# Performance work log

Hardware: AMD Instinct MI355X
Metric: run time of the kernel (lower is better)

## Reference

```python
import jax, jax.numpy as jnp
import numpy as np

N_NODES = 40000
N_EDGES = 640000
D = 128  # in_channels == out_channels (required by the module's math)


def setup_inputs() -> dict:
    key = jax.random.key(0)
    ks = jax.random.split(key, 8)
    s = 1.0 / np.sqrt(D)  # torch Linear default init scale
    x = jax.random.normal(ks[0], (N_NODES, D), dtype=jnp.float32)
    edge_index = jax.random.randint(ks[1], (2, N_EDGES), 0, N_NODES, dtype=jnp.int64)
    Wn_w = jax.random.uniform(ks[2], (D, D), jnp.float32, -s, s)
    Wn_b = jax.random.uniform(ks[3], (D,), jnp.float32, -s, s)
    Wg_w = jax.random.uniform(ks[4], (D, D), jnp.float32, -s, s)
    Wg_b = jax.random.uniform(ks[5], (D,), jnp.float32, -s, s)
    Wa_w = jax.random.uniform(ks[6], (D, D), jnp.float32, -s, s)
    Wa_b = jax.random.uniform(ks[7], (D,), jnp.float32, -s, s)
    return {"x": x, "edge_index": edge_index,
            "Wn_w": Wn_w, "Wn_b": Wn_b,
            "Wg_w": Wg_w, "Wg_b": Wg_b,
            "Wa_w": Wa_w, "Wa_b": Wa_b}


def reference(x, edge_index, Wn_w, Wn_b, Wg_w, Wg_b, Wa_w, Wa_b):
    row, col = edge_index[0], edge_index[1]
    x_col = x[col]                                  # [E, D] gather
    alpha = jax.nn.sigmoid(x_col @ Wa_w + Wa_b)     # [E, D] edge attention
    neigh = x_col * alpha                           # [E, D]
    aggr = jax.ops.segment_sum(neigh, row, num_segments=x.shape[0])  # [N, D]
    out = jnp.tanh((x @ Wn_w + Wn_b) + (aggr @ Wg_w + Wg_b))
    return out  # dropout p=0.0 is identity
```

## Files before the change

kernel.cpp:

```cpp
#include <hip/hip_runtime.h>

#define NN 40000
#define NE 640000
#define D 128
#define CAP 64

typedef __attribute__((ext_vector_type(8))) short short8;
typedef __attribute__((ext_vector_type(4))) float f32x4;
typedef __attribute__((ext_vector_type(4))) int i32x4;

__device__ __forceinline__ short f2b(float v) {
  unsigned int u = __builtin_bit_cast(unsigned int, v);
  u = (u + 0x7fffu + ((u >> 16) & 1u)) >> 16;
  return (short)u;
}
__device__ __forceinline__ float b2f(short s) {
  unsigned int u = ((unsigned int)(unsigned short)s) << 16;
  return __builtin_bit_cast(float, u);
}

__global__ __launch_bounds__(256) void k_prep(
    const float* __restrict__ Wn, const float* __restrict__ Wg,
    const float* __restrict__ Wa, short* __restrict__ WnT,
    short* __restrict__ WgThi, short* __restrict__ WgTlo,
    short* __restrict__ WaT, int* __restrict__ cnt, short* __restrict__ h) {
  int i = blockIdx.x * 256 + threadIdx.x;
  int k = i >> 7, c = i & 127;
  WnT[c * D + k] = f2b(Wn[k * D + c]);
  WaT[c * D + k] = f2b(Wa[k * D + c]);
  float v = Wg[k * D + c];
  short hi = f2b(v);
  WgThi[c * D + k] = hi;
  WgTlo[c * D + k] = f2b(v - b2f(hi));
  if (i < 10000) {
    i32x4 z = {0, 0, 0, 0};
    *(i32x4*)(cnt + i * 4) = z;
  }
  if (i < 16) {
    short8 z = {0, 0, 0, 0, 0, 0, 0, 0};
    *(short8*)(h + (size_t)NN * D + i * 8) = z;
  }
}

__global__ __launch_bounds__(256) void k_fill(
    const int* __restrict__ ei, int* __restrict__ cnt,
    unsigned short* __restrict__ bucket) {
  int e = blockIdx.x * 256 + threadIdx.x;
  if (e >= NE) return;
  int r = ei[e];
  int c = ei[NE + e];
  int slot = atomicAdd(&cnt[r], 1);
  if (slot < CAP) bucket[(size_t)r * CAP + slot] = (unsigned short)c;
}

__global__ __launch_bounds__(256) void k_node(
    const float* __restrict__ x, const short* __restrict__ WaT,
    const float* __restrict__ ba, short* __restrict__ h_out,
    short* __restrict__ xbf_out) {
  __shared__ float xs[16][132];
  __shared__ float al_s[16][132];
  int r0 = blockIdx.x * 16;
  int t = threadIdx.x;
  int w = t >> 6, l = t & 63;
  int g = l >> 4, c16 = l & 15;

#pragma unroll
  for (int p = 0; p < 2; ++p) {
    int idx = t + p * 256;
    int row = idx >> 5, cv = idx & 31;
    f32x4 v = *(const f32x4*)(x + (size_t)(r0 + row) * D + cv * 4);
    *(f32x4*)&xs[row][cv * 4] = v;
  }
  __syncthreads();

  short8 a[4];
#pragma unroll
  for (int kt = 0; kt < 4; ++kt) {
    f32x4 v0 = *(const f32x4*)&xs[c16][kt * 32 + g * 8];
    f32x4 v1 = *(const f32x4*)&xs[c16][kt * 32 + g * 8 + 4];
    short8 tt;
    tt[0] = f2b(v0[0]); tt[1] = f2b(v0[1]); tt[2] = f2b(v0[2]); tt[3] = f2b(v0[3]);
    tt[4] = f2b(v1[0]); tt[5] = f2b(v1[1]); tt[6] = f2b(v1[2]); tt[7] = f2b(v1[3]);
    a[kt] = tt;
    *(short8*)(xbf_out + (size_t)(r0 + c16) * D + kt * 32 + g * 8) = tt;
  }

#pragma unroll
  for (int u = 0; u < 2; ++u) {
    int ct = w * 2 + u;
    int cc = ct * 16 + c16;
    f32x4 c = {0.f, 0.f, 0.f, 0.f};
#pragma unroll
    for (int kt = 0; kt < 4; ++kt) {
      short8 b = *(const short8*)(WaT + (size_t)cc * D + kt * 32 + g * 8);
      c = __builtin_amdgcn_mfma_f32_16x16x32_bf16(a[kt], b, c, 0, 0, 0);
    }
    float bav = ba[cc];
#pragma unroll
    for (int r = 0; r < 4; ++r) {
      float tv = c[r] + bav;
      al_s[g * 4 + r][cc] = 1.0f / (1.0f + __expf(-tv));
    }
  }
  __syncthreads();

  short8 hh;
#pragma unroll
  for (int q = 0; q < 8; ++q) {
    float av = al_s[c16][w * 32 + g * 8 + q];
    float xv = xs[c16][w * 32 + g * 8 + q];
    hh[q] = f2b(xv * av);
  }
  *(short8*)(h_out + (size_t)(r0 + c16) * D + w * 32 + g * 8) = hh;
}

#define PSTEP(T0, C0A, C0B, C1A, C1B)                               \
  {                                                                 \
    int s0 = 4 * (T0) + g, s1 = s0 + 4;                             \
    int ra0 = s0 < deg0 ? (C0A) : NN;                               \
    int ra1 = s1 < deg0 ? (C0B) : NN;                               \
    int rb0 = s0 < deg1 ? (C1A) : NN;                               \
    int rb1 = s1 < deg1 ? (C1B) : NN;                               \
    short8 va0 = *(const short8*)(h + (size_t)ra0 * D + i * 8);     \
    short8 va1 = *(const short8*)(h + (size_t)ra1 * D + i * 8);     \
    short8 vb0 = *(const short8*)(h + (size_t)rb0 * D + i * 8);     \
    short8 vb1 = *(const short8*)(h + (size_t)rb1 * D + i * 8);     \
    _Pragma("unroll") for (int q = 0; q < 8; ++q) {                 \
      a0[q] += b2f(va0[q]) + b2f(va1[q]);                           \
      a1[q] += b2f(vb0[q]) + b2f(vb1[q]);                           \
    }                                                               \
  }

__global__ __launch_bounds__(512) void k_fused(
    const int* __restrict__ cnt, const unsigned short* __restrict__ bucket,
    const short* __restrict__ h, const short* __restrict__ xbf,
    const short* __restrict__ WnT, const short* __restrict__ WgThi,
    const short* __restrict__ WgTlo, const float* __restrict__ bn,
    const float* __restrict__ bg, float* __restrict__ out) {
  __shared__ float st[16][132];
  __shared__ short xsb[16][132];
  int w = threadIdx.x >> 6, l = threadIdx.x & 63;
  int g = l >> 4, i = l & 15;
  int base = blockIdx.x * 16;

  if (threadIdx.x < 256) {
    int idx = threadIdx.x;
    int row = idx >> 4, ch = idx & 15;
    *(short8*)&xsb[row][ch * 8] =
        *(const short8*)(xbf + (size_t)(base + row) * D + ch * 8);
  }

  {
    int n0 = base + 2 * w, n1 = n0 + 1;
    int deg0 = cnt[n0]; deg0 = deg0 < CAP ? deg0 : CAP;
    int deg1 = cnt[n1]; deg1 = deg1 < CAP ? deg1 : CAP;
    int dmax = deg0 > deg1 ? deg0 : deg1;
    int bc0 = bucket[(size_t)n0 * CAP + l];
    int bc1 = bucket[(size_t)n1 * CAP + l];
    float a0[8], a1[8];
#pragma unroll
    for (int q = 0; q < 8; ++q) { a0[q] = 0.f; a1[q] = 0.f; }

    int c00 = __shfl(bc0, g), c01 = __shfl(bc0, 4 + g);
    int c02 = __shfl(bc0, 8 + g), c03 = __shfl(bc0, 12 + g);
    int c10 = __shfl(bc1, g), c11 = __shfl(bc1, 4 + g);
    int c12 = __shfl(bc1, 8 + g), c13 = __shfl(bc1, 12 + g);
    PSTEP(0, c00, c01, c10, c11);
    if (dmax > 8) PSTEP(2, c02, c03, c12, c13);
    if (dmax > 16) {
      int c04 = __shfl(bc0, 16 + g), c05 = __shfl(bc0, 20 + g);
      int c14 = __shfl(bc1, 16 + g), c15 = __shfl(bc1, 20 + g);
      PSTEP(4, c04, c05, c14, c15);
    }
    if (dmax > 24) {
      int c06 = __shfl(bc0, 24 + g), c07 = __shfl(bc0, 28 + g);
      int c16_ = __shfl(bc1, 24 + g), c17 = __shfl(bc1, 28 + g);
      PSTEP(6, c06, c07, c16_, c17);
    }
    if (dmax > 32) {
      for (int j = 32; j < dmax; j += 8) {
        int s0 = j + g, s1 = j + 4 + g;
        int d00 = __shfl(bc0, s0 & 63), d01 = __shfl(bc0, s1 & 63);
        int d10 = __shfl(bc1, s0 & 63), d11 = __shfl(bc1, s1 & 63);
        int ra0 = s0 < deg0 ? d00 : NN;
        int ra1 = s1 < deg0 ? d01 : NN;
        int rb0 = s0 < deg1 ? d10 : NN;
        int rb1 = s1 < deg1 ? d11 : NN;
        short8 va0 = *(const short8*)(h + (size_t)ra0 * D + i * 8);
        short8 va1 = *(const short8*)(h + (size_t)ra1 * D + i * 8);
        short8 vb0 = *(const short8*)(h + (size_t)rb0 * D + i * 8);
        short8 vb1 = *(const short8*)(h + (size_t)rb1 * D + i * 8);
#pragma unroll
        for (int q = 0; q < 8; ++q) {
          a0[q] += b2f(va0[q]) + b2f(va1[q]);
          a1[q] += b2f(vb0[q]) + b2f(vb1[q]);
        }
      }
    }
#pragma unroll
    for (int q = 0; q < 8; ++q) {
      a0[q] += __shfl_xor(a0[q], 16);
      a0[q] += __shfl_xor(a0[q], 32);
      a1[q] += __shfl_xor(a1[q], 16);
      a1[q] += __shfl_xor(a1[q], 32);
    }
    if (g == 0) {
      f32x4 lo = {a0[0], a0[1], a0[2], a0[3]};
      f32x4 hi = {a0[4], a0[5], a0[6], a0[7]};
      *(f32x4*)&st[w * 2][i * 8] = lo;
      *(f32x4*)&st[w * 2][i * 8 + 4] = hi;
    } else if (g == 1) {
      f32x4 lo = {a1[0], a1[1], a1[2], a1[3]};
      f32x4 hi = {a1[4], a1[5], a1[6], a1[7]};
      *(f32x4*)&st[w * 2 + 1][i * 8] = lo;
      *(f32x4*)&st[w * 2 + 1][i * 8 + 4] = hi;
    }
  }
  __syncthreads();

  int cc = w * 16 + i;
  f32x4 c = {0.f, 0.f, 0.f, 0.f};
  float bias = bn[cc] + bg[cc];
#pragma unroll
  for (int kt = 0; kt < 4; ++kt) {
    short8 axf = *(const short8*)&xsb[i][kt * 32 + g * 8];
    const float* p = &st[i][kt * 32 + g * 8];
    f32x4 v0 = *(const f32x4*)p;
    f32x4 v1 = *(const f32x4*)(p + 4);
    short8 sh, sl;
#pragma unroll
    for (int jq = 0; jq < 4; ++jq) {
      short hh = f2b(v0[jq]);
      sh[jq] = hh;
      sl[jq] = f2b(v0[jq] - b2f(hh));
    }
#pragma unroll
    for (int jq = 0; jq < 4; ++jq) {
      short hh = f2b(v1[jq]);
      sh[4 + jq] = hh;
      sl[4 + jq] = f2b(v1[jq] - b2f(hh));
    }
    short8 bwn = *(const short8*)(WnT + (size_t)cc * D + kt * 32 + g * 8);
    short8 bh = *(const short8*)(WgThi + (size_t)cc * D + kt * 32 + g * 8);
    short8 bl = *(const short8*)(WgTlo + (size_t)cc * D + kt * 32 + g * 8);
    c = __builtin_amdgcn_mfma_f32_16x16x32_bf16(axf, bwn, c, 0, 0, 0);
    c = __builtin_amdgcn_mfma_f32_16x16x32_bf16(sh, bh, c, 0, 0, 0);
    c = __builtin_amdgcn_mfma_f32_16x16x32_bf16(sl, bh, c, 0, 0, 0);
    c = __builtin_amdgcn_mfma_f32_16x16x32_bf16(sh, bl, c, 0, 0, 0);
  }
#pragma unroll
  for (int r = 0; r < 4; ++r) {
    int rr = base + g * 4 + r;
    out[(size_t)rr * D + cc] = tanhf(c[r] + bias);
  }
}

extern "C" void kernel_launch(void* const* d_in, const int* in_sizes, int n_in,
                              void* d_out, int out_size, void* d_ws,
                              size_t ws_size, hipStream_t stream) {
  const float* x = (const float*)d_in[0];
  const int* ei = (const int*)d_in[1];
  const float* Wn_w = (const float*)d_in[2];
  const float* Wn_b = (const float*)d_in[3];
  const float* Wg_w = (const float*)d_in[4];
  const float* Wg_b = (const float*)d_in[5];
  const float* Wa_w = (const float*)d_in[6];
  const float* Wa_b = (const float*)d_in[7];

  char* ws = (char*)d_ws;
  short* WaT = (short*)(ws + 0);
  short* WnT = (short*)(ws + 32 * 1024);
  short* WgThi = (short*)(ws + 64 * 1024);
  short* WgTlo = (short*)(ws + 96 * 1024);
  int* cnt = (int*)(ws + 128 * 1024);
  size_t off = 512 * 1024;
  short* h = (short*)(ws + off);
  off += (size_t)(NN + 1) * D * 2;
  short* xbf = (short*)(ws + off);
  off += (size_t)NN * D * 2;
  unsigned short* bucket = (unsigned short*)(ws + off);
  float* out = (float*)d_out;

  k_prep<<<64, 256, 0, stream>>>(Wn_w, Wg_w, Wa_w, WnT, WgThi, WgTlo, WaT,
                                 cnt, h);
  k_fill<<<(NE + 255) / 256, 256, 0, stream>>>(ei, cnt, bucket);
  k_node<<<NN / 16, 256, 0, stream>>>(x, WaT, Wa_b, h, xbf);
  k_fused<<<2500, 512, 0, stream>>>(cnt, bucket, h, xbf, WnT, WgThi, WgTlo,
                                    Wn_b, Wg_b, out);
}
```

Baseline: 107.0 us.

## Double rows per block with dynamic node-pair scheduling across waves

Each block of k_fused now handles 32 nodes instead of 16. Waves pull node pairs from a shared atomic counter, so uneven node degrees are balanced within the block instead of each wave owning a fixed pair. The epilogue is restructured so each wave computes two 16-column tiles for one 16-row tile, reusing the converted A fragments across both. This halves the block count and adds LDS atomics, and the larger LDS footprint may lower occupancy.

```diff
diff --git a/kernel.cpp b/kernel.cpp
--- a/kernel.cpp
+++ b/kernel.cpp
@@ -137,21 +137,24 @@
     const short* __restrict__ WnT, const short* __restrict__ WgThi,
     const short* __restrict__ WgTlo, const float* __restrict__ bn,
     const float* __restrict__ bg, float* __restrict__ out) {
-  __shared__ float st[16][132];
-  __shared__ short xsb[16][132];
+  __shared__ float st[32][132];
+  __shared__ short xsb[32][132];
+  __shared__ int nxt;
   int w = threadIdx.x >> 6, l = threadIdx.x & 63;
   int g = l >> 4, i = l & 15;
-  int base = blockIdx.x * 16;
-
-  if (threadIdx.x < 256) {
-    int idx = threadIdx.x;
-    int row = idx >> 4, ch = idx & 15;
+  int base = blockIdx.x * 32;
+
+  {
+    int row = threadIdx.x >> 4, ch = threadIdx.x & 15;
     *(short8*)&xsb[row][ch * 8] =
         *(const short8*)(xbf + (size_t)(base + row) * D + ch * 8);
   }
-
-  {
-    int n0 = base + 2 * w, n1 = n0 + 1;
+  if (threadIdx.x == 0) nxt = 8;
+  __syncthreads();
+
+  int p = w;
+  while (true) {
+    int n0 = base + 2 * p, n1 = n0 + 1;
     int deg0 = cnt[n0]; deg0 = deg0 < CAP ? deg0 : CAP;
     int deg1 = cnt[n1]; deg1 = deg1 < CAP ? deg1 : CAP;
     int dmax = deg0 > deg1 ? deg0 : deg1;
@@ -207,51 +210,69 @@
     if (g == 0) {
       f32x4 lo = {a0[0], a0[1], a0[2], a0[3]};
       f32x4 hi = {a0[4], a0[5], a0[6], a0[7]};
-      *(f32x4*)&st[w * 2][i * 8] = lo;
-      *(f32x4*)&st[w * 2][i * 8 + 4] = hi;
+      *(f32x4*)&st[2 * p][i * 8] = lo;
+      *(f32x4*)&st[2 * p][i * 8 + 4] = hi;
     } else if (g == 1) {
       f32x4 lo = {a1[0], a1[1], a1[2], a1[3]};
       f32x4 hi = {a1[4], a1[5], a1[6], a1[7]};
-      *(f32x4*)&st[w * 2 + 1][i * 8] = lo;
-      *(f32x4*)&st[w * 2 + 1][i * 8 + 4] = hi;
-    }
+      *(f32x4*)&st[2 * p + 1][i * 8] = lo;
+      *(f32x4*)&st[2 * p + 1][i * 8 + 4] = hi;
+    }
+    int np;
+    if (l == 0) np = atomicAdd(&nxt, 1);
+    np = __shfl(np, 0);
+    if (np >= 16) break;
+    p = np;
   }
   __syncthreads();
 
-  int cc = w * 16 + i;
-  f32x4 c = {0.f, 0.f, 0.f, 0.f};
-  float bias = bn[cc] + bg[cc];
+  int rt = w & 1, ci = w >> 1;
+  int rl = rt * 16 + i;
+  short8 axf[4], sh[4], sl[4];
 #pragma unroll
   for (int kt = 0; kt < 4; ++kt) {
-    short8 axf = *(const short8*)&xsb[i][kt * 32 + g * 8];
-    const float* p = &st[i][kt * 32 + g * 8];
-    f32x4 v0 = *(const f32x4*)p;
-    f32x4 v1 = *(const f32x4*)(p + 4);
-    short8 sh, sl;
+    axf[kt] = *(const short8*)&xsb[rl][kt * 32 + g * 8];
+    const float* pp = &st[rl][kt * 32 + g * 8];
+    f32x4 v0 = *(const f32x4*)pp;
+    f32x4 v1 = *(const f32x4*)(pp + 4);
+    short8 th, tl;
 #pragma unroll
     for (int jq = 0; jq < 4; ++jq) {
       short hh = f2b(v0[jq]);
-      sh[jq] = hh;
-      sl[jq] = f2b(v0[jq] - b2f(hh));
+      th[jq] = hh;
+      tl[jq] = f2b(v0[jq] - b2f(hh));
     }
 #pragma unroll
     for (int jq = 0; jq < 4; ++jq) {
       short hh = f2b(v1[jq]);
-      sh[4 + jq] = hh;
-      sl[4 + jq] = f2b(v1[jq] - b2f(hh));
-    }
-    short8 bwn = *(const short8*)(WnT + (size_t)cc * D + kt * 32 + g * 8);
-    short8 bh = *(const short8*)(WgThi + (size_t)cc * D + kt * 32 + g * 8);
-    short8 bl = *(const short8*)(WgTlo + (size_t)cc * D + kt * 32 + g * 8);
-    c = __builtin_amdgcn_mfma_f32_16x16x32_bf16(axf, bwn, c, 0, 0, 0);
-    c = __builtin_amdgcn_mfma_f32_16x16x32_bf16(sh, bh, c, 0, 0, 0);
-    c = __builtin_amdgcn_mfma_f32_16x16x32_bf16(sl, bh, c, 0, 0, 0);
-    c = __builtin_amdgcn_mfma_f32_16x16x32_bf16(sh, bl, c, 0, 0, 0);
-  }
-#pragma unroll
-  for (int r = 0; r < 4; ++r) {
-    int rr = base + g * 4 + r;
-    out[(size_t)rr * D + cc] = tanhf(c[r] + bias);
+      th[4 + jq] = hh;
+      tl[4 + jq] = f2b(v1[jq] - b2f(hh));
+    }
+    sh[kt] = th;
+    sl[kt] = tl;
+  }
+
+#pragma unroll
+  for (int u = 0; u < 2; ++u) {
+    int ct = ci * 2 + u;
+    int cc = ct * 16 + i;
+    f32x4 c = {0.f, 0.f, 0.f, 0.f};
+#pragma unroll
+    for (int kt = 0; kt < 4; ++kt) {
+      short8 bwn = *(const short8*)(WnT + (size_t)cc * D + kt * 32 + g * 8);
+      short8 bh = *(const short8*)(WgThi + (size_t)cc * D + kt * 32 + g * 8);
+      short8 bl = *(const short8*)(WgTlo + (size_t)cc * D + kt * 32 + g * 8);
+      c = __builtin_amdgcn_mfma_f32_16x16x32_bf16(axf[kt], bwn, c, 0, 0, 0);
+      c = __builtin_amdgcn_mfma_f32_16x16x32_bf16(sh[kt], bh, c, 0, 0, 0);
+      c = __builtin_amdgcn_mfma_f32_16x16x32_bf16(sl[kt], bh, c, 0, 0, 0);
+      c = __builtin_amdgcn_mfma_f32_16x16x32_bf16(sh[kt], bl, c, 0, 0, 0);
+    }
+    float bias = bn[cc] + bg[cc];
+#pragma unroll
+    for (int r = 0; r < 4; ++r) {
+      int rr = base + rt * 16 + g * 4 + r;
+      out[(size_t)rr * D + cc] = tanhf(c[r] + bias);
+    }
   }
 }
 
@@ -285,6 +306,6 @@
                                  cnt, h);
   k_fill<<<(NE + 255) / 256, 256, 0, stream>>>(ei, cnt, bucket);
   k_node<<<NN / 16, 256, 0, stream>>>(x, WaT, Wa_b, h, xbf);
-  k_fused<<<2500, 512, 0, stream>>>(cnt, bucket, h, xbf, WnT, WgThi, WgTlo,
-                                    Wn_b, Wg_b, out);
-}
+  k_fused<<<NN / 32, 512, 0, stream>>>(cnt, bucket, h, xbf, WnT, WgThi,
+                                       WgTlo, Wn_b, Wg_b, out);
+}
```

Measured after the change: 120.8 us. +13.0%, slower.

## Merge edge bucketing into node kernel and pre-split aggregate into bf16 hi/lo

Applied to the files above, without the earlier changes.

Merges the edge-bucketing kernel into the per-node attention kernel by giving the extra 2500 blocks the bucket-fill role, which removes one launch and lets the two independent workloads run concurrently. In the fused kernel, the aggregated sums are split into packed bf16 hi/lo pairs once, before they are written to shared memory, rather than every consumer lane converting fp32 again. The dense matmul chain is split into two independent MFMA accumulators so the Wn and Wg chains can overlap. The risks are more register pressure and a mixed block workload in the merged kernel.

```diff
diff --git a/kernel.cpp b/kernel.cpp
--- a/kernel.cpp
+++ b/kernel.cpp
@@ -42,24 +42,23 @@
   }
 }
 
-__global__ __launch_bounds__(256) void k_fill(
-    const int* __restrict__ ei, int* __restrict__ cnt,
-    unsigned short* __restrict__ bucket) {
-  int e = blockIdx.x * 256 + threadIdx.x;
-  if (e >= NE) return;
-  int r = ei[e];
-  int c = ei[NE + e];
-  int slot = atomicAdd(&cnt[r], 1);
-  if (slot < CAP) bucket[(size_t)r * CAP + slot] = (unsigned short)c;
-}
-
-__global__ __launch_bounds__(256) void k_node(
+__global__ __launch_bounds__(256) void k_nf(
     const float* __restrict__ x, const short* __restrict__ WaT,
     const float* __restrict__ ba, short* __restrict__ h_out,
-    short* __restrict__ xbf_out) {
+    short* __restrict__ xbf_out, const int* __restrict__ ei,
+    int* __restrict__ cnt, unsigned short* __restrict__ bucket) {
+  int bid = blockIdx.x;
+  if (bid >= 2500) {
+    int e = (bid - 2500) * 256 + threadIdx.x;
+    int r = ei[e];
+    int c = ei[NE + e];
+    int slot = atomicAdd(&cnt[r], 1);
+    if (slot < CAP) bucket[(size_t)r * CAP + slot] = (unsigned short)c;
+    return;
+  }
   __shared__ float xs[16][132];
   __shared__ float al_s[16][132];
-  int r0 = blockIdx.x * 16;
+  int r0 = bid * 16;
   int t = threadIdx.x;
   int w = t >> 6, l = t & 63;
   int g = l >> 4, c16 = l & 15;
@@ -137,15 +136,14 @@
     const short* __restrict__ WnT, const short* __restrict__ WgThi,
     const short* __restrict__ WgTlo, const float* __restrict__ bn,
     const float* __restrict__ bg, float* __restrict__ out) {
-  __shared__ float st[16][132];
+  __shared__ unsigned int st[16][132];
   __shared__ short xsb[16][132];
   int w = threadIdx.x >> 6, l = threadIdx.x & 63;
   int g = l >> 4, i = l & 15;
   int base = blockIdx.x * 16;
 
   if (threadIdx.x < 256) {
-    int idx = threadIdx.x;
-    int row = idx >> 4, ch = idx & 15;
+    int row = threadIdx.x >> 4, ch = threadIdx.x & 15;
     *(short8*)&xsb[row][ch * 8] =
         *(const short8*)(xbf + (size_t)(base + row) * D + ch * 8);
   }
@@ -205,53 +203,59 @@
       a1[q] += __shfl_xor(a1[q], 32);
     }
     if (g == 0) {
-      f32x4 lo = {a0[0], a0[1], a0[2], a0[3]};
-      f32x4 hi = {a0[4], a0[5], a0[6], a0[7]};
-      *(f32x4*)&st[w * 2][i * 8] = lo;
-      *(f32x4*)&st[w * 2][i * 8 + 4] = hi;
+      unsigned int u[8];
+#pragma unroll
+      for (int q = 0; q < 8; ++q) {
+        short hi = f2b(a0[q]);
+        short lo = f2b(a0[q] - b2f(hi));
+        u[q] = ((unsigned int)(unsigned short)hi << 16) | (unsigned short)lo;
+      }
+      *(i32x4*)&st[2 * w][i * 8] = *(i32x4*)&u[0];
+      *(i32x4*)&st[2 * w][i * 8 + 4] = *(i32x4*)&u[4];
     } else if (g == 1) {
-      f32x4 lo = {a1[0], a1[1], a1[2], a1[3]};
-      f32x4 hi = {a1[4], a1[5], a1[6], a1[7]};
-      *(f32x4*)&st[w * 2 + 1][i * 8] = lo;
-      *(f32x4*)&st[w * 2 + 1][i * 8 + 4] = hi;
+      unsigned int u[8];
+#pragma unroll
+      for (int q = 0; q < 8; ++q) {
+        short hi = f2b(a1[q]);
+        short lo = f2b(a1[q] - b2f(hi));
+        u[q] = ((unsigned int)(unsigned short)hi << 16) | (unsigned short)lo;
+      }
+      *(i32x4*)&st[2 * w + 1][i * 8] = *(i32x4*)&u[0];
+      *(i32x4*)&st[2 * w + 1][i * 8 + 4] = *(i32x4*)&u[4];
     }
   }
   __syncthreads();
 
   int cc = w * 16 + i;
-  f32x4 c = {0.f, 0.f, 0.f, 0.f};
-  float bias = bn[cc] + bg[cc];
+  f32x4 cn = {0.f, 0.f, 0.f, 0.f};
+  f32x4 cg = {0.f, 0.f, 0.f, 0.f};
 #pragma unroll
   for (int kt = 0; kt < 4; ++kt) {
     short8 axf = *(const short8*)&xsb[i][kt * 32 + g * 8];
-    const float* p = &st[i][kt * 32 + g * 8];
-    f32x4 v0 = *(const f32x4*)p;
-    f32x4 v1 = *(const f32x4*)(p + 4);
-    short8 sh, sl;
-#pragma unroll
-    for (int jq = 0; jq < 4; ++jq) {
-      short hh = f2b(v0[jq]);
-      sh[jq] = hh;
-      sl[jq] = f2b(v0[jq] - b2f(hh));
-    }
-#pragma unroll
-    for (int jq = 0; jq < 4; ++jq) {
-      short hh = f2b(v1[jq]);
-      sh[4 + jq] = hh;
-      sl[4 + jq] = f2b(v1[jq] - b2f(hh));
+    i32x4 u0 = *(const i32x4*)&st[i][kt * 32 + g * 8];
+    i32x4 u1 = *(const i32x4*)&st[i][kt * 32 + g * 8 + 4];
+    short8 shf, slf;
+#pragma unroll
+    for (int q = 0; q < 4; ++q) {
+      unsigned int ua = (unsigned int)u0[q], ub = (unsigned int)u1[q];
+      shf[q] = (short)(ua >> 16);
+      slf[q] = (short)(ua & 0xffffu);
+      shf[4 + q] = (short)(ub >> 16);
+      slf[4 + q] = (short)(ub & 0xffffu);
     }
     short8 bwn = *(const short8*)(WnT + (size_t)cc * D + kt * 32 + g * 8);
     short8 bh = *(const short8*)(WgThi + (size_t)cc * D + kt * 32 + g * 8);
     short8 bl = *(const short8*)(WgTlo + (size_t)cc * D + kt * 32 + g * 8);
-    c = __builtin_amdgcn_mfma_f32_16x16x32_bf16(axf, bwn, c, 0, 0, 0);
-    c = __builtin_amdgcn_mfma_f32_16x16x32_bf16(sh, bh, c, 0, 0, 0);
-    c = __builtin_amdgcn_mfma_f32_16x16x32_bf16(sl, bh, c, 0, 0, 0);
-    c = __builtin_amdgcn_mfma_f32_16x16x32_bf16(sh, bl, c, 0, 0, 0);
-  }
+    cn = __builtin_amdgcn_mfma_f32_16x16x32_bf16(axf, bwn, cn, 0, 0, 0);
+    cg = __builtin_amdgcn_mfma_f32_16x16x32_bf16(shf, bh, cg, 0, 0, 0);
+    cg = __builtin_amdgcn_mfma_f32_16x16x32_bf16(slf, bh, cg, 0, 0, 0);
+    cg = __builtin_amdgcn_mfma_f32_16x16x32_bf16(shf, bl, cg, 0, 0, 0);
+  }
+  float bias = bn[cc] + bg[cc];
 #pragma unroll
   for (int r = 0; r < 4; ++r) {
     int rr = base + g * 4 + r;
-    out[(size_t)rr * D + cc] = tanhf(c[r] + bias);
+    out[(size_t)rr * D + cc] = tanhf(cn[r] + cg[r] + bias);
   }
 }
 
@@ -283,8 +287,7 @@
 
   k_prep<<<64, 256, 0, stream>>>(Wn_w, Wg_w, Wa_w, WnT, WgThi, WgTlo, WaT,
                                  cnt, h);
-  k_fill<<<(NE + 255) / 256, 256, 0, stream>>>(ei, cnt, bucket);
-  k_node<<<NN / 16, 256, 0, stream>>>(x, WaT, Wa_b, h, xbf);
+  k_nf<<<5000, 256, 0, stream>>>(x, WaT, Wa_b, h, xbf, ei, cnt, bucket);
   k_fused<<<2500, 512, 0, stream>>>(cnt, bucket, h, xbf, WnT, WgThi, WgTlo,
                                     Wn_b, Wg_b, out);
 }
```

Result: slower. 126.6 us (+18.3%).
